# Kernel optimization log

Hardware: AMD Instinct MI355X
Metric: run time of the kernel (lower is better)

The kernel has to match this reference:

```python
import jax, jax.numpy as jnp
import numpy as np

WIN = (7, 7)
N_TOK = WIN[0] * WIN[1]          # 49
DIM = 512
HEADS = 16
B_WIN = 2048                     # num_windows * batch
NW = 64                          # windows per image (mask leading dim)


def _relative_position_index():
    # Mirrors the torch __init__ coords computation.
    coords = np.stack(np.meshgrid(np.arange(WIN[0]), np.arange(WIN[1]), indexing='ij'))  # [2,Wh,Ww]
    flat = coords.reshape(2, -1)                                   # [2, N]
    rel = flat[:, :, None] - flat[:, None, :]                      # [2, N, N]
    rel = rel.transpose(1, 2, 0).astype(np.int32)                  # [N, N, 2]
    rel[:, :, 0] += WIN[0] - 1
    rel[:, :, 1] += WIN[1] - 1
    rel[:, :, 0] *= 2 * WIN[1] - 1
    return jnp.asarray(rel.sum(-1), dtype=jnp.int32)               # [N, N]


def setup_inputs() -> dict:
    key = jax.random.key(0)
    ks = jax.random.split(key, 7)
    x = jax.random.normal(ks[0], (B_WIN, N_TOK, DIM), jnp.float32)
    w_qkv = jax.random.normal(ks[1], (3 * DIM, DIM), jnp.float32) * 0.02
    b_qkv = jax.random.normal(ks[2], (3 * DIM,), jnp.float32) * 0.02
    w_proj = jax.random.normal(ks[3], (DIM, DIM), jnp.float32) * 0.02
    b_proj = jax.random.normal(ks[4], (DIM,), jnp.float32) * 0.02
    bias_table = jax.random.normal(ks[5], ((2 * WIN[0] - 1) * (2 * WIN[1] - 1), HEADS), jnp.float32) * 0.02
    rel_index = _relative_position_index()
    # shift-window mask: 0 for allowed, -100 for masked (Swin convention)
    mask = jnp.where(jax.random.bernoulli(ks[6], 0.1, (NW, N_TOK, N_TOK)), -100.0, 0.0).astype(jnp.float32)
    return {"x": x, "w_qkv": w_qkv, "b_qkv": b_qkv, "w_proj": w_proj,
            "b_proj": b_proj, "bias_table": bias_table, "rel_index": rel_index, "mask": mask}


def reference(x, w_qkv, b_qkv, w_proj, b_proj, bias_table, rel_index, mask):
    B_, N, C = x.shape
    H = HEADS
    hd = C // H
    scale = hd ** -0.5
    # qkv projection: [B, N, 3, H, hd] -> q,k,v each [B, H, N, hd]
    qkv = (jnp.einsum('bnc,oc->bno', x, w_qkv) + b_qkv)
    qkv = qkv.reshape(B_, N, 3, H, hd).transpose(2, 0, 3, 1, 4)
    q, k, v = qkv[0], qkv[1], qkv[2]
    attn = jnp.einsum('bhnd,bhmd->bhnm', q * scale, k)             # [B, H, N, N]
    # relative position bias gather: [N*N] -> [N, N, H] -> [H, N, N]
    rpb = bias_table[rel_index.reshape(-1)].reshape(N, N, H).transpose(2, 0, 1)
    attn = attn + rpb[None]
    nW = mask.shape[0]
    attn = attn.reshape(B_ // nW, nW, H, N, N) + mask[None, :, None]
    attn = attn.reshape(B_, H, N, N)
    attn = jax.nn.softmax(attn, axis=-1)
    out = jnp.einsum('bhnm,bhmd->bhnd', attn, v)                   # [B, H, N, hd]
    out = out.transpose(0, 2, 1, 3).reshape(B_, N, C)
    out = jnp.einsum('bnc,oc->bno', out, w_proj) + b_proj
    return out
```

## Files before the change

kernel.cpp:

```cpp
#include <hip/hip_runtime.h>
#include <stdint.h>

typedef unsigned short u16;
typedef unsigned int u32;
typedef __attribute__((ext_vector_type(4))) u16 u16x4;
typedef __attribute__((ext_vector_type(8))) u16 u16x8;
typedef __attribute__((ext_vector_type(2))) u32 u32x2;
typedef __attribute__((ext_vector_type(8))) short bf16x8;
typedef __attribute__((ext_vector_type(4))) float f32x4;

#define DEVFN __device__ __forceinline__

DEVFN u16 f2bf(float f) {
  union { float f; u32 u; } x; x.f = f;
  u32 u = x.u;
  return (u16)((u + 0x7fffu + ((u >> 16) & 1u)) >> 16);
}

__global__ void cvt_kernel(const float* __restrict__ in, u16* __restrict__ out, int n4) {
  const int stride = gridDim.x * blockDim.x;
  for (int i = blockIdx.x * blockDim.x + threadIdx.x; i < n4; i += stride) {
    float4 v = reinterpret_cast<const float4*>(in)[i];
    u16x4 o;
    o.x = f2bf(v.x); o.y = f2bf(v.y); o.z = f2bf(v.z); o.w = f2bf(v.w);
    reinterpret_cast<u16x4*>(out)[i] = o;
  }
}

__global__ void pbp_kernel(const float* __restrict__ bt, const int* __restrict__ ri,
                           float* __restrict__ pbp) {
  const int h = blockIdx.x;
  for (int t = threadIdx.x; t < 4096; t += 256) {
    const int i = t >> 6, j = t & 63;
    float v = 0.f;
    if (i < 49 && j < 49) v = bt[ri[i * 49 + j] * 16 + h];
    pbp[h * 4096 + t] = v;
  }
}

__global__ void maskp_kernel(const float* __restrict__ mask, float* __restrict__ maskp) {
  const int w = blockIdx.x;
  for (int t = threadIdx.x; t < 4096; t += 256) {
    const int i = t >> 6, j = t & 63;
    float v = -1e30f;
    if (i < 49 && j < 49) v = mask[w * 2401 + i * 49 + j];
    maskp[w * 4096 + t] = v;
  }
}

#define WAIT_LGKM0 asm volatile("s_waitcnt lgkmcnt(0)" ::: "memory")
#define WAIT_VM8   asm volatile("s_waitcnt vmcnt(8)" ::: "memory")
#define WAIT_VM0   asm volatile("s_waitcnt vmcnt(0)" ::: "memory")
#define SCHEDB     __builtin_amdgcn_sched_barrier(0)
#define BARRIER    __builtin_amdgcn_s_barrier()

template <int MODE, int NTILES, int MCHUNK>
__global__ __launch_bounds__(256) void gemm_kernel(
    const u16* __restrict__ A, const u16* __restrict__ Bt,
    const float* __restrict__ bias, void* __restrict__ Out, int ldo) {
  __shared__ u16 sA[2][128 * 64];
  __shared__ u16 sB[2][128 * 64];
  const int tid = threadIdx.x;
  const int lane = tid & 63;
  const int wid = tid >> 6;
  const int bid = blockIdx.x;
  const int xcd = bid & 7;
  const int slot = bid >> 3;
  const int m0 = (xcd * MCHUNK + slot / NTILES) * 128;
  const int n0 = (slot % NTILES) * 128;
  const int wr = wid >> 1, wc = wid & 1;
  const int l15 = lane & 15, lg = lane >> 4;
  const int sr = lane >> 3;
  const int ss = lane & 7;

#define STAGE(kt, bufi)                                                        \
  {                                                                            \
    _Pragma("unroll") for (int i = 0; i < 4; ++i) {                            \
      const int r = wid * 32 + i * 8 + sr;                                     \
      const int srcs = ss ^ (r & 7);                                           \
      const u16* ga = A + (size_t)(m0 + r) * 512 + (kt) * 64 + srcs * 8;       \
      const u16* gb = Bt + (size_t)(n0 + r) * 512 + (kt) * 64 + srcs * 8;      \
      __builtin_amdgcn_global_load_lds(                                        \
          (const __attribute__((address_space(1))) void*)ga,                   \
          (__attribute__((address_space(3))) void*)(sA[bufi] +                 \
                                                    (wid * 32 + i * 8) * 64),  \
          16, 0, 0);                                                           \
      __builtin_amdgcn_global_load_lds(                                        \
          (const __attribute__((address_space(1))) void*)gb,                   \
          (__attribute__((address_space(3))) void*)(sB[bufi] +                 \
                                                    (wid * 32 + i * 8) * 64),  \
          16, 0, 0);                                                           \
    }                                                                          \
  }

  f32x4 acc[4][4] = {};

  STAGE(0, 0);
  STAGE(1, 1);
  WAIT_VM8;
  BARRIER;
  SCHEDB;

#pragma unroll
  for (int t = 0; t < 8; ++t) {
    const int cur = t & 1;
    bf16x8 af[2][4], bfr[2][4];
#pragma unroll
    for (int ks = 0; ks < 2; ++ks) {
#pragma unroll
      for (int mi = 0; mi < 4; ++mi) {
        const int m = wr * 64 + mi * 16 + l15;
        const int slotm = (ks * 4 + lg) ^ (m & 7);
        af[ks][mi] = *reinterpret_cast<const bf16x8*>(sA[cur] + m * 64 + slotm * 8);
      }
#pragma unroll
      for (int ni = 0; ni < 4; ++ni) {
        const int n = wc * 64 + ni * 16 + l15;
        const int slotn = (ks * 4 + lg) ^ (n & 7);
        bfr[ks][ni] = *reinterpret_cast<const bf16x8*>(sB[cur] + n * 64 + slotn * 8);
      }
    }
    WAIT_LGKM0;
    SCHEDB;
    BARRIER;
    SCHEDB;
    if (t < 6) STAGE(t + 2, cur);
    __builtin_amdgcn_s_setprio(1);
#pragma unroll
    for (int ks = 0; ks < 2; ++ks)
#pragma unroll
      for (int mi = 0; mi < 4; ++mi)
#pragma unroll
        for (int ni = 0; ni < 4; ++ni)
          acc[mi][ni] = __builtin_amdgcn_mfma_f32_16x16x32_bf16(af[ks][mi], bfr[ks][ni], acc[mi][ni], 0, 0, 0);
    __builtin_amdgcn_s_setprio(0);
    SCHEDB;
    if (t < 6) {
      WAIT_VM8;
    } else if (t == 6) {
      WAIT_VM0;
    }
    if (t < 7) {
      BARRIER;
      SCHEDB;
    }
  }
#undef STAGE

#pragma unroll
  for (int mi = 0; mi < 4; ++mi) {
#pragma unroll
    for (int ni = 0; ni < 4; ++ni) {
      const int col = n0 + wc * 64 + ni * 16 + l15;
      const float bv = bias[col];
      const int rbase = m0 + wr * 64 + mi * 16 + lg * 4;
#pragma unroll
      for (int r = 0; r < 4; ++r) {
        const float v = acc[mi][ni][r] + bv;
        if (MODE == 0) {
          ((u16*)Out)[(size_t)(rbase + r) * ldo + col] = f2bf(v);
        } else {
          ((float*)Out)[(size_t)(rbase + r) * ldo + col] = v;
        }
      }
    }
  }
}

__global__ __launch_bounds__(256) void attn_kernel(
    const u16* __restrict__ qkv, const float* __restrict__ pbp,
    const float* __restrict__ maskp, u16* __restrict__ attn_out) {
  const int w = threadIdx.x >> 6;
  const int lane = threadIdx.x & 63;
  const int b = blockIdx.x >> 2;
  const int h = ((blockIdx.x & 3) << 2) | w;
  const int l15 = lane & 15, lg = lane >> 4;

  __shared__ u16 sVT[4][32][72];
  u16 (*vt)[72] = sVT[w];

  for (int i = lane; i < 1152; i += 64) ((u32*)vt)[i] = 0;

  const size_t rowbase = (size_t)b * (49 * 1536) + h * 32;

  for (int c = lane; c < 196; c += 64) {
    const int n = c >> 2, dg = c & 3;
    u16x8 vv = *reinterpret_cast<const u16x8*>(qkv + rowbase + (size_t)n * 1536 + 1024 + dg * 8);
    const int pin = ((n >> 5) << 5) | ((((n >> 2) & 3)) << 3) | (((n >> 4) & 1) << 2) | (n & 3);
#pragma unroll
    for (int j = 0; j < 8; ++j) vt[dg * 8 + j][pin] = vv[j];
  }

  bf16x8 aq[4], bk[4];
#pragma unroll
  for (int t = 0; t < 4; ++t) {
    const int i = t * 16 + l15;
    const int r = i < 49 ? i : 48;
    const size_t ro = rowbase + (size_t)r * 1536 + lg * 8;
    aq[t] = *reinterpret_cast<const bf16x8*>(qkv + ro);
    bk[t] = *reinterpret_cast<const bf16x8*>(qkv + ro + 512);
  }

  bf16x8 bv[2][2];
#pragma unroll
  for (int ni = 0; ni < 2; ++ni)
#pragma unroll
    for (int ks = 0; ks < 2; ++ks)
      bv[ni][ks] = *reinterpret_cast<const bf16x8*>(&vt[ni * 16 + l15][ks * 32 + lg * 8]);

  const float scale = 0.17677669529663687f;
  const float* pbh = pbp + (h << 12);
  const float* mw = maskp + ((size_t)(b & 63) << 12);
  const size_t obase = (size_t)b * 49 * 512 + h * 32;

#pragma unroll
  for (int qt = 0; qt < 4; ++qt) {
    f32x4 sT[4] = {};
#pragma unroll
    for (int kt = 0; kt < 4; ++kt)
      sT[kt] = __builtin_amdgcn_mfma_f32_16x16x32_bf16(bk[kt], aq[qt], sT[kt], 0, 0, 0);

    const int i = qt * 16 + l15;
    const float* pr = pbh + i * 64 + lg * 4;
    const float* mr = mw + i * 64 + lg * 4;
    float v[4][4];
    float mx = -3e38f;
#pragma unroll
    for (int kt = 0; kt < 4; ++kt) {
      f32x4 pv = *reinterpret_cast<const f32x4*>(pr + kt * 16);
      f32x4 mv = *reinterpret_cast<const f32x4*>(mr + kt * 16);
#pragma unroll
      for (int r = 0; r < 4; ++r) {
        const float val = fmaf(sT[kt][r], scale, pv[r] + mv[r]);
        v[kt][r] = val;
        mx = fmaxf(mx, val);
      }
    }
    mx = fmaxf(mx, __shfl_xor(mx, 16));
    mx = fmaxf(mx, __shfl_xor(mx, 32));
    float sum = 0.f;
#pragma unroll
    for (int kt = 0; kt < 4; ++kt)
#pragma unroll
      for (int r = 0; r < 4; ++r) {
        const float e = __expf(v[kt][r] - mx);
        v[kt][r] = e;
        sum += e;
      }
    sum += __shfl_xor(sum, 16);
    sum += __shfl_xor(sum, 32);
    const float rinv = 1.0f / sum;

    bf16x8 ap[2];
#pragma unroll
    for (int ks = 0; ks < 2; ++ks) {
      u32 w0 = (u32)f2bf(v[2 * ks][0] * rinv) | ((u32)f2bf(v[2 * ks][1] * rinv) << 16);
      u32 w1 = (u32)f2bf(v[2 * ks][2] * rinv) | ((u32)f2bf(v[2 * ks][3] * rinv) << 16);
      u32 w2 = (u32)f2bf(v[2 * ks + 1][0] * rinv) | ((u32)f2bf(v[2 * ks + 1][1] * rinv) << 16);
      u32 w3 = (u32)f2bf(v[2 * ks + 1][2] * rinv) | ((u32)f2bf(v[2 * ks + 1][3] * rinv) << 16);
      union { u32 u[4]; bf16x8 b; } pk;
      pk.u[0] = w0; pk.u[1] = w1; pk.u[2] = w2; pk.u[3] = w3;
      ap[ks] = pk.b;
    }

    f32x4 o[2] = {};
#pragma unroll
    for (int ks = 0; ks < 2; ++ks)
#pragma unroll
      for (int ni = 0; ni < 2; ++ni)
        o[ni] = __builtin_amdgcn_mfma_f32_16x16x32_bf16(ap[ks], bv[ni][ks], o[ni], 0, 0, 0);

#pragma unroll
    for (int r = 0; r < 4; ++r) {
      const int iq = qt * 16 + lg * 4 + r;
      if (iq < 49) {
#pragma unroll
        for (int ni = 0; ni < 2; ++ni)
          attn_out[obase + (size_t)iq * 512 + ni * 16 + l15] = f2bf(o[ni][r]);
      }
    }
  }
}

extern "C" void kernel_launch(void* const* d_in, const int* in_sizes, int n_in,
                              void* d_out, int out_size, void* d_ws, size_t ws_size,
                              hipStream_t stream) {
  (void)in_sizes; (void)n_in; (void)out_size; (void)ws_size;
  const float* x          = (const float*)d_in[0];
  const float* w_qkv      = (const float*)d_in[1];
  const float* b_qkv      = (const float*)d_in[2];
  const float* w_proj     = (const float*)d_in[3];
  const float* b_proj     = (const float*)d_in[4];
  const float* bias_table = (const float*)d_in[5];
  const int*   rel_index  = (const int*)d_in[6];
  const float* mask       = (const float*)d_in[7];

  u16* ws     = (u16*)d_ws;
  u16* xbf    = ws;
  u16* qkv    = ws + 51380224;
  u16* wqkvb  = qkv + 154140672;
  u16* wprojb = wqkvb + 786432;
  float* pbp  = (float*)(wprojb + 262144);
  float* mkp  = pbp + 16 * 4096;

  cvt_kernel<<<2048, 256, 0, stream>>>(x, xbf, 51380224 / 4);
  cvt_kernel<<<192, 256, 0, stream>>>(w_qkv, wqkvb, 786432 / 4);
  cvt_kernel<<<64, 256, 0, stream>>>(w_proj, wprojb, 262144 / 4);
  pbp_kernel<<<16, 256, 0, stream>>>(bias_table, rel_index, pbp);
  maskp_kernel<<<64, 256, 0, stream>>>(mask, mkp);

  gemm_kernel<0, 12, 98><<<9408, 256, 0, stream>>>(xbf, wqkvb, b_qkv, qkv, 1536);
  attn_kernel<<<8192, 256, 0, stream>>>(qkv, pbp, mkp, xbf);
  gemm_kernel<1, 4, 98><<<3136, 256, 0, stream>>>(xbf, wprojb, b_proj, d_out, 512);
}
```

Before: 628.5 us.

## Enlarge GEMM tiles to 256x256 with 8 waves and interleaved LDS reads

Both projection GEMMs move from 128x128 tiles with 4 waves to 256x256 tiles with 8 waves, using 128 KB of dynamic shared memory for double buffering. Each wave now computes a 128x64 sub-tile, and its LDS fragment reads are split into four phases interleaved with MFMA groups, with the next-stage prefetch issued mid-iteration. The aim is more reuse per loaded byte and better overlap of LDS reads with MFMA work. The cost is one block per CU due to the LDS footprint, higher register pressure from 32 accumulators, and fewer blocks (784) for the output projection.

```diff
diff --git a/kernel.cpp b/kernel.cpp
--- a/kernel.cpp
+++ b/kernel.cpp
@@ -53,107 +53,149 @@
 #define WAIT_VM0   asm volatile("s_waitcnt vmcnt(0)" ::: "memory")
 #define SCHEDB     __builtin_amdgcn_sched_barrier(0)
 #define BARRIER    __builtin_amdgcn_s_barrier()
+#define MFMA(a, b, c) __builtin_amdgcn_mfma_f32_16x16x32_bf16(a, b, c, 0, 0, 0)
 
 template <int MODE, int NTILES, int MCHUNK>
-__global__ __launch_bounds__(256) void gemm_kernel(
+__global__ __launch_bounds__(512) void gemm_kernel(
     const u16* __restrict__ A, const u16* __restrict__ Bt,
     const float* __restrict__ bias, void* __restrict__ Out, int ldo) {
-  __shared__ u16 sA[2][128 * 64];
-  __shared__ u16 sB[2][128 * 64];
+  extern __shared__ u16 smem[];
   const int tid = threadIdx.x;
   const int lane = tid & 63;
   const int wid = tid >> 6;
   const int bid = blockIdx.x;
   const int xcd = bid & 7;
   const int slot = bid >> 3;
-  const int m0 = (xcd * MCHUNK + slot / NTILES) * 128;
-  const int n0 = (slot % NTILES) * 128;
-  const int wr = wid >> 1, wc = wid & 1;
+  const int m0 = (xcd * MCHUNK + slot / NTILES) * 256;
+  const int n0 = (slot % NTILES) * 256;
+  const int wr = wid >> 2, wc = wid & 3;
   const int l15 = lane & 15, lg = lane >> 4;
-  const int sr = lane >> 3;
-  const int ss = lane & 7;
-
-#define STAGE(kt, bufi)                                                        \
+  const int rg0 = tid >> 3;
+  const int sl0 = tid & 7;
+
+  f32x4 acc[8][4] = {};
+
+  u16* const sA0 = smem;
+  u16* const sB0 = smem + 16384;
+  u16* const sA1 = smem + 32768;
+  u16* const sB1 = smem + 49152;
+
+#define STAGE(kt_, sa_, sb_)                                                   \
   {                                                                            \
     _Pragma("unroll") for (int i = 0; i < 4; ++i) {                            \
-      const int r = wid * 32 + i * 8 + sr;                                     \
-      const int srcs = ss ^ (r & 7);                                           \
-      const u16* ga = A + (size_t)(m0 + r) * 512 + (kt) * 64 + srcs * 8;       \
-      const u16* gb = Bt + (size_t)(n0 + r) * 512 + (kt) * 64 + srcs * 8;      \
+      const int rg = i * 64 + rg0;                                             \
+      const int kc = sl0 ^ (rg & 7);                                           \
+      const u16* ga = A + (size_t)(m0 + rg) * 512 + (kt_) * 64 + kc * 8;       \
       __builtin_amdgcn_global_load_lds(                                        \
           (const __attribute__((address_space(1))) void*)ga,                   \
-          (__attribute__((address_space(3))) void*)(sA[bufi] +                 \
-                                                    (wid * 32 + i * 8) * 64),  \
+          (__attribute__((address_space(3))) void*)((sa_) + i * 4096 + wid * 512), \
           16, 0, 0);                                                           \
+    }                                                                          \
+    _Pragma("unroll") for (int i = 0; i < 4; ++i) {                            \
+      const int rg = i * 64 + rg0;                                             \
+      const int kc = sl0 ^ (rg & 7);                                           \
+      const u16* gb = Bt + (size_t)(n0 + rg) * 512 + (kt_) * 64 + kc * 8;      \
       __builtin_amdgcn_global_load_lds(                                        \
           (const __attribute__((address_space(1))) void*)gb,                   \
-          (__attribute__((address_space(3))) void*)(sB[bufi] +                 \
-                                                    (wid * 32 + i * 8) * 64),  \
+          (__attribute__((address_space(3))) void*)((sb_) + i * 4096 + wid * 512), \
           16, 0, 0);                                                           \
     }                                                                          \
   }
 
-  f32x4 acc[4][4] = {};
-
-  STAGE(0, 0);
-  STAGE(1, 1);
-  WAIT_VM8;
-  BARRIER;
-  SCHEDB;
-
-#pragma unroll
-  for (int t = 0; t < 8; ++t) {
-    const int cur = t & 1;
-    bf16x8 af[2][4], bfr[2][4];
-#pragma unroll
-    for (int ks = 0; ks < 2; ++ks) {
-#pragma unroll
-      for (int mi = 0; mi < 4; ++mi) {
-        const int m = wr * 64 + mi * 16 + l15;
-        const int slotm = (ks * 4 + lg) ^ (m & 7);
-        af[ks][mi] = *reinterpret_cast<const bf16x8*>(sA[cur] + m * 64 + slotm * 8);
-      }
-#pragma unroll
-      for (int ni = 0; ni < 4; ++ni) {
-        const int n = wc * 64 + ni * 16 + l15;
-        const int slotn = (ks * 4 + lg) ^ (n & 7);
-        bfr[ks][ni] = *reinterpret_cast<const bf16x8*>(sB[cur] + n * 64 + slotn * 8);
-      }
-    }
-    WAIT_LGKM0;
+#define RDA(dst, sa_, mi, ks)                                                  \
+  {                                                                            \
+    const int row_ = wr * 128 + (mi) * 16 + l15;                               \
+    dst = *reinterpret_cast<const bf16x8*>(                                    \
+        (sa_) + row_ * 64 + ((((ks) * 4 + lg) ^ (row_ & 7)) << 3));            \
+  }
+#define RDB(dst, sb_, ni, ks)                                                  \
+  {                                                                            \
+    const int row_ = wc * 64 + (ni) * 16 + l15;                                \
+    dst = *reinterpret_cast<const bf16x8*>(                                    \
+        (sb_) + row_ * 64 + ((((ks) * 4 + lg) ^ (row_ & 7)) << 3));            \
+  }
+
+  STAGE(0, sA0, sB0);
+  STAGE(1, sA1, sB1);
+  WAIT_VM8; SCHEDB;
+  BARRIER; SCHEDB;
+
+#pragma unroll
+  for (int kt = 0; kt < 8; ++kt) {
+    u16* const sa = (kt & 1) ? sA1 : sA0;
+    u16* const sb = (kt & 1) ? sB1 : sB0;
+    bf16x8 a0[4][2], a1[4][2], b0[2][2], b1[2][2];
+
+#pragma unroll
+    for (int mi = 0; mi < 4; ++mi) { RDA(a0[mi][0], sa, mi, 0); RDA(a0[mi][1], sa, mi, 1); }
+#pragma unroll
+    for (int ni = 0; ni < 2; ++ni) { RDB(b0[ni][0], sb, ni, 0); RDB(b0[ni][1], sb, ni, 1); }
+    WAIT_LGKM0; SCHEDB;
+    __builtin_amdgcn_s_setprio(1);
+#pragma unroll
+    for (int mi = 0; mi < 4; ++mi)
+#pragma unroll
+      for (int ni = 0; ni < 2; ++ni)
+#pragma unroll
+        for (int ks = 0; ks < 2; ++ks)
+          acc[mi][ni] = MFMA(a0[mi][ks], b0[ni][ks], acc[mi][ni]);
+    __builtin_amdgcn_s_setprio(0); SCHEDB;
+
+#pragma unroll
+    for (int ni = 0; ni < 2; ++ni) { RDB(b1[ni][0], sb, ni + 2, 0); RDB(b1[ni][1], sb, ni + 2, 1); }
+    WAIT_LGKM0; SCHEDB;
+    __builtin_amdgcn_s_setprio(1);
+#pragma unroll
+    for (int mi = 0; mi < 4; ++mi)
+#pragma unroll
+      for (int ni = 0; ni < 2; ++ni)
+#pragma unroll
+        for (int ks = 0; ks < 2; ++ks)
+          acc[mi][ni + 2] = MFMA(a0[mi][ks], b1[ni][ks], acc[mi][ni + 2]);
+    __builtin_amdgcn_s_setprio(0); SCHEDB;
+
+#pragma unroll
+    for (int mi = 0; mi < 4; ++mi) { RDA(a1[mi][0], sa, mi + 4, 0); RDA(a1[mi][1], sa, mi + 4, 1); }
+    WAIT_LGKM0; SCHEDB;
+    __builtin_amdgcn_s_setprio(1);
+#pragma unroll
+    for (int mi = 0; mi < 4; ++mi)
+#pragma unroll
+      for (int ni = 0; ni < 2; ++ni)
+#pragma unroll
+        for (int ks = 0; ks < 2; ++ks)
+          acc[mi + 4][ni + 2] = MFMA(a1[mi][ks], b1[ni][ks], acc[mi + 4][ni + 2]);
+    __builtin_amdgcn_s_setprio(0); SCHEDB;
+
+    BARRIER; SCHEDB;
+    if (kt < 6) STAGE(kt + 2, sa, sb);
+
+    __builtin_amdgcn_s_setprio(1);
+#pragma unroll
+    for (int mi = 0; mi < 4; ++mi)
+#pragma unroll
+      for (int ni = 0; ni < 2; ++ni)
+#pragma unroll
+        for (int ks = 0; ks < 2; ++ks)
+          acc[mi + 4][ni] = MFMA(a1[mi][ks], b0[ni][ks], acc[mi + 4][ni]);
+    __builtin_amdgcn_s_setprio(0); SCHEDB;
+
+    if (kt < 6) { WAIT_VM8; }
+    else if (kt == 6) { WAIT_VM0; }
     SCHEDB;
-    BARRIER;
-    SCHEDB;
-    if (t < 6) STAGE(t + 2, cur);
-    __builtin_amdgcn_s_setprio(1);
-#pragma unroll
-    for (int ks = 0; ks < 2; ++ks)
-#pragma unroll
-      for (int mi = 0; mi < 4; ++mi)
-#pragma unroll
-        for (int ni = 0; ni < 4; ++ni)
-          acc[mi][ni] = __builtin_amdgcn_mfma_f32_16x16x32_bf16(af[ks][mi], bfr[ks][ni], acc[mi][ni], 0, 0, 0);
-    __builtin_amdgcn_s_setprio(0);
-    SCHEDB;
-    if (t < 6) {
-      WAIT_VM8;
-    } else if (t == 6) {
-      WAIT_VM0;
-    }
-    if (t < 7) {
-      BARRIER;
-      SCHEDB;
-    }
+    if (kt < 7) { BARRIER; SCHEDB; }
   }
 #undef STAGE
-
-#pragma unroll
-  for (int mi = 0; mi < 4; ++mi) {
+#undef RDA
+#undef RDB
+
+#pragma unroll
+  for (int mi = 0; mi < 8; ++mi) {
 #pragma unroll
     for (int ni = 0; ni < 4; ++ni) {
       const int col = n0 + wc * 64 + ni * 16 + l15;
       const float bv = bias[col];
-      const int rbase = m0 + wr * 64 + mi * 16 + lg * 4;
+      const int rbase = m0 + wr * 128 + mi * 16 + lg * 4;
 #pragma unroll
       for (int r = 0; r < 4; ++r) {
         const float v = acc[mi][ni][r] + bv;
@@ -303,13 +345,18 @@
   float* pbp  = (float*)(wprojb + 262144);
   float* mkp  = pbp + 16 * 4096;
 
+  (void)hipFuncSetAttribute((const void*)gemm_kernel<0, 6, 49>,
+                            hipFuncAttributeMaxDynamicSharedMemorySize, 131072);
+  (void)hipFuncSetAttribute((const void*)gemm_kernel<1, 2, 49>,
+                            hipFuncAttributeMaxDynamicSharedMemorySize, 131072);
+
   cvt_kernel<<<2048, 256, 0, stream>>>(x, xbf, 51380224 / 4);
   cvt_kernel<<<192, 256, 0, stream>>>(w_qkv, wqkvb, 786432 / 4);
   cvt_kernel<<<64, 256, 0, stream>>>(w_proj, wprojb, 262144 / 4);
   pbp_kernel<<<16, 256, 0, stream>>>(bias_table, rel_index, pbp);
   maskp_kernel<<<64, 256, 0, stream>>>(mask, mkp);
 
-  gemm_kernel<0, 12, 98><<<9408, 256, 0, stream>>>(xbf, wqkvb, b_qkv, qkv, 1536);
+  gemm_kernel<0, 6, 49><<<2352, 512, 131072, stream>>>(xbf, wqkvb, b_qkv, qkv, 1536);
   attn_kernel<<<8192, 256, 0, stream>>>(qkv, pbp, mkp, xbf);
-  gemm_kernel<1, 4, 98><<<3136, 256, 0, stream>>>(xbf, wprojb, b_proj, d_out, 512);
-}
+  gemm_kernel<1, 2, 49><<<784, 512, 131072, stream>>>(xbf, wprojb, b_proj, d_out, 512);
+}
```

Result: faster. 568.3 us (-9.6%).
